# Kernel tuning notes

Measured on AMD Instinct MI355X. Metric: run time of the kernel, lower is better.

## Reference

```python
import jax, jax.numpy as jnp
import numpy as np

B = 500_000
N = 6          # n_neurons
STEPS = 10     # spiking update loop length
SUBSTEPS = 8   # TwoCompColumn substeps
NOISE_STD = 0.3
I_TONIC = -1.0
# Izhikevich 'RS' parameters
IZ_A, IZ_B, IZ_C, IZ_D = 0.02, 0.2, -65.0, 8.0
V_THRESH = 30.0
RATE_ALPHA = 0.1   # rate EMA
PC_TAU = 0.5       # compartment relaxation rate


def setup_inputs() -> dict:
    key = jax.random.key(0)
    k = jax.random.split(key, 8)
    heading = jax.random.normal(k[0], (B,), dtype=jnp.float32)
    speed = jax.random.uniform(k[1], (B,), dtype=jnp.float32)
    turn_rate = jax.random.normal(k[2], (B,), dtype=jnp.float32)
    predicted_turn = jax.random.normal(k[3], (B,), dtype=jnp.float32)
    predicted_speed = jax.random.uniform(k[4], (B,), dtype=jnp.float32)
    noise = jax.random.normal(k[5], (STEPS, B, N), dtype=jnp.float32)
    # Izhikevich resting state around v=-65, u=b*v, with small jitter
    v0 = -65.0 + 2.0 * jax.random.normal(k[6], (B, N), dtype=jnp.float32)
    u0 = IZ_B * v0
    rate0 = jnp.zeros((B, N), dtype=jnp.float32)
    return {
        "heading": heading, "speed": speed, "turn_rate": turn_rate,
        "predicted_turn": predicted_turn, "predicted_speed": predicted_speed,
        "noise": noise, "v0": v0, "u0": u0, "rate0": rate0,
    }


def reference(heading, speed, turn_rate, predicted_turn, predicted_speed,
              noise, v0, u0, rate0):
    # heading is carried for API fidelity; original forward never uses it.
    del heading
    tilt = jnp.minimum(1.0, jnp.abs(turn_rate) * speed * 0.5)          # [B]
    zero = jnp.float32(0.0)
    I = jnp.stack([
        jnp.maximum(zero, turn_rate) * 10.0,
        jnp.maximum(zero, -turn_rate) * 10.0,
        speed * 5.0,
        jnp.maximum(zero, -speed + 0.5) * 5.0,
        tilt * 8.0,
        tilt * 8.0,
    ], axis=-1)                                                        # [B, N]

    def izh_step(carry, nz):
        v, u, r = carry                                                # each [B, N]
        i_tot = I + nz * NOISE_STD + I_TONIC
        v = v + (0.04 * v * v + 5.0 * v + 140.0 - u + i_tot)
        u = u + IZ_A * (IZ_B * v - u)
        fired = v >= V_THRESH
        spk = fired.astype(v.dtype)
        v = jnp.where(fired, IZ_C, v)
        u = u + spk * IZ_D
        r = r * (1.0 - RATE_ALPHA) + spk * RATE_ALPHA
        return (v, u, r), None

    (_, _, rate), _ = jax.lax.scan(izh_step, (v0, u0, rate0), noise)
    rate_mean = jnp.mean(rate, axis=-1)                                # [B]

    # TwoCompColumn: basal tracks sensory, apical tracks prediction
    sensory = jnp.stack([turn_rate, speed], axis=-1)                   # [B, 2]
    prediction = jnp.stack([predicted_turn, predicted_speed], axis=-1) # [B, 2]

    def pc_step(carry, _):
        vb, va = carry
        vb = vb + PC_TAU * (sensory - vb)
        va = va + PC_TAU * (prediction - va)
        return (vb, va), None

    (vb, va), _ = jax.lax.scan(pc_step,
                               (jnp.zeros_like(sensory), jnp.zeros_like(prediction)),
                               None, length=SUBSTEPS)
    pe = vb - va                                                       # [B, 2]
    precision = 1.0 / (1.0 + pe * pe)                                  # [B, 2]
    free_energy = 0.5 * jnp.sum(precision * pe * pe, axis=-1)          # [B]
    pe_w = 0.7 * pe[..., 0] + 0.3 * pe[..., 1]                         # [B]
    prec_mean = jnp.mean(precision, axis=-1)                           # [B]
    postural = -prec_mean * pe_w * 0.3                                 # [B]

    # [B, 6]: (tilt, rate, postural_correction, prediction_error, precision, free_energy)
    return jnp.stack([tilt, rate_mean, postural, pe_w, prec_mean, free_energy], axis=-1)
```

## Files before the change

kernel.cpp:

```cpp
#include <hip/hip_runtime.h>

#define STEPS 10

__global__ __launch_bounds__(256) void spiking_vestibular_kernel(
    const float* __restrict__ speed,
    const float* __restrict__ turn_rate,
    const float* __restrict__ predicted_turn,
    const float* __restrict__ predicted_speed,
    const float* __restrict__ noise,
    const float* __restrict__ v0,
    const float* __restrict__ u0,
    const float* __restrict__ rate0,
    float* __restrict__ out,
    int B)
{
#pragma clang fp contract(off)
    int tid = blockIdx.x * blockDim.x + threadIdx.x;
    int b = tid >> 2;
    int g = tid & 3;
    if (b >= B) return;

    size_t base6 = (size_t)b * 6;
    int goff = (g == 3) ? 0 : (2 * g);

    float2 nz[STEPS];
#pragma unroll
    for (int t = 0; t < STEPS; ++t)
        nz[t] = *reinterpret_cast<const float2*>(noise + (size_t)t * (size_t)B * 6 + base6 + goff);

    float2 v2 = *reinterpret_cast<const float2*>(v0    + base6 + goff);
    float2 u2 = *reinterpret_cast<const float2*>(u0    + base6 + goff);
    float2 r2 = *reinterpret_cast<const float2*>(rate0 + base6 + goff);

    float tr = turn_rate[b];
    float sp = speed[b];
    float pt = predicted_turn[b];
    float ps = predicted_speed[b];

    float tilt = fminf(1.0f, (fabsf(tr) * sp) * 0.5f);

    float t8 = tilt * 8.0f;
    float Ia = (g == 0) ? fmaxf(0.0f, tr) * 10.0f
             : (g == 1) ? sp * 5.0f
             : t8;
    float Ib = (g == 0) ? fmaxf(0.0f, -tr) * 10.0f
             : (g == 1) ? fmaxf(0.0f, -sp + 0.5f) * 5.0f
             : t8;

    float va = v2.x, vb = v2.y;
    float ua = u2.x, ub = u2.y;
    float ra = r2.x, rb = r2.y;

#pragma unroll
    for (int t = 0; t < STEPS; ++t) {
        {
            float i_tot = Ia + nz[t].x * 0.3f + (-1.0f);
            float vv = va, un = ua;
            vv = vv + (((((0.04f * vv) * vv) + (5.0f * vv)) + 140.0f) - un + i_tot);
            un = un + 0.02f * ((0.2f * vv) - un);
            bool fired = (vv >= 30.0f);
            float spk = fired ? 1.0f : 0.0f;
            vv = fired ? -65.0f : vv;
            un = un + spk * 8.0f;
            ra = ra * 0.9f + spk * 0.1f;
            va = vv; ua = un;
        }
        {
            float i_tot = Ib + nz[t].y * 0.3f + (-1.0f);
            float vv = vb, un = ub;
            vv = vv + (((((0.04f * vv) * vv) + (5.0f * vv)) + 140.0f) - un + i_tot);
            un = un + 0.02f * ((0.2f * vv) - un);
            bool fired = (vv >= 30.0f);
            float spk = fired ? 1.0f : 0.0f;
            vv = fired ? -65.0f : vv;
            un = un + spk * 8.0f;
            rb = rb * 0.9f + spk * 0.1f;
            vb = vv; ub = un;
        }
    }

    float s  = ra + rb;
    float s1 = __shfl_down(s, 1, 4);
    float s2 = __shfl_down(s, 2, 4);
    float rate_mean = ((s + s1) + s2) / 6.0f;

    float cb0 = 0.0f, cb1 = 0.0f, ca0 = 0.0f, ca1 = 0.0f;
#pragma unroll
    for (int k = 0; k < 8; ++k) {
        cb0 = cb0 + 0.5f * (tr - cb0);
        cb1 = cb1 + 0.5f * (sp - cb1);
        ca0 = ca0 + 0.5f * (pt - ca0);
        ca1 = ca1 + 0.5f * (ps - ca1);
    }
    float pe0 = cb0 - ca0;
    float pe1 = cb1 - ca1;
    float prec0 = 1.0f / (1.0f + pe0 * pe0);
    float prec1 = 1.0f / (1.0f + pe1 * pe1);
    float fe = 0.5f * (((prec0 * pe0) * pe0) + ((prec1 * pe1) * pe1));
    float pe_w = 0.7f * pe0 + 0.3f * pe1;
    float prec_mean = (prec0 + prec1) / 2.0f;
    float postural = (-prec_mean) * pe_w * 0.3f;

    if (g < 3) {
        float2 o = (g == 0) ? make_float2(tilt, rate_mean)
                 : (g == 1) ? make_float2(postural, pe_w)
                 :            make_float2(prec_mean, fe);
        *reinterpret_cast<float2*>(out + base6 + 2 * g) = o;
    }
}

extern "C" void kernel_launch(void* const* d_in, const int* in_sizes, int n_in,
                              void* d_out, int out_size, void* d_ws, size_t ws_size,
                              hipStream_t stream) {
    const float* speed           = (const float*)d_in[1];
    const float* turn_rate       = (const float*)d_in[2];
    const float* predicted_turn  = (const float*)d_in[3];
    const float* predicted_speed = (const float*)d_in[4];
    const float* noise           = (const float*)d_in[5];
    const float* v0              = (const float*)d_in[6];
    const float* u0              = (const float*)d_in[7];
    const float* rate0           = (const float*)d_in[8];
    float* out                   = (float*)d_out;

    int B = in_sizes[1];
    long long total = (long long)B * 4;
    int block = 256;
    int grid = (int)((total + block - 1) / block);
    spiking_vestibular_kernel<<<grid, block, 0, stream>>>(
        speed, turn_rate, predicted_turn, predicted_speed,
        noise, v0, u0, rate0, out, B);
}
```

Measured before the change: 219.2 us.

## Stage noise and state slabs into LDS via direct global-to-LDS loads

```diff
diff --git a/kernel.cpp b/kernel.cpp
--- a/kernel.cpp
+++ b/kernel.cpp
@@ -1,6 +1,14 @@
 #include <hip/hip_runtime.h>
 
 #define STEPS 10
+#define EPB 64
+#define SLAB_FLOATS 384
+#define LDS_FLOATS 5120
+
+#define GLOAD_LDS16(gp, lp)                                            \
+    __builtin_amdgcn_global_load_lds(                                  \
+        (const __attribute__((address_space(1))) void*)(gp),           \
+        (__attribute__((address_space(3))) void*)(lp), 16, 0, 0)
 
 __global__ __launch_bounds__(256) void spiking_vestibular_kernel(
     const float* __restrict__ speed,
@@ -15,22 +23,51 @@
     int B)
 {
 #pragma clang fp contract(off)
-    int tid = blockIdx.x * blockDim.x + threadIdx.x;
-    int b = tid >> 2;
-    int g = tid & 3;
+    __shared__ float smem[LDS_FLOATS];
+
+    const int tid  = threadIdx.x;
+    const int wave = tid >> 6;
+    const int lane = tid & 63;
+    const long long b0 = (long long)blockIdx.x * EPB;
+
+    const long long nz_lim = (long long)STEPS * B * 6 - 4;
+    const long long st_lim = (long long)B * 6 - 4;
+
+#pragma unroll
+    for (int r = 0; r < 5; ++r) {
+        const int c = r * 4 + wave;
+        const int k = (c << 6) | lane;
+        int s = k / 96;
+        const int off16 = k - s * 96;
+        if (s > 12) s = 0;
+        const float* basep;
+        long long fidx, lim;
+        if (s < 10)       { basep = noise; fidx = ((long long)s * B + b0) * 6; lim = nz_lim; }
+        else if (s == 10) { basep = v0;    fidx = b0 * 6; lim = st_lim; }
+        else if (s == 11) { basep = u0;    fidx = b0 * 6; lim = st_lim; }
+        else              { basep = rate0; fidx = b0 * 6; lim = st_lim; }
+        fidx += (long long)off16 * 4;
+        if (fidx > lim) fidx = lim;
+        GLOAD_LDS16(basep + fidx, &smem[c * 256]);
+    }
+
+    __syncthreads();
+
+    const int e = tid >> 2;
+    const int g = tid & 3;
+    const long long b = b0 + e;
     if (b >= B) return;
 
-    size_t base6 = (size_t)b * 6;
-    int goff = (g == 3) ? 0 : (2 * g);
+    const int goff = (g == 3) ? 0 : (2 * g);
+    const int sb = e * 6 + goff;
 
-    float2 nz[STEPS];
+    float2 nzv[STEPS];
 #pragma unroll
     for (int t = 0; t < STEPS; ++t)
-        nz[t] = *reinterpret_cast<const float2*>(noise + (size_t)t * (size_t)B * 6 + base6 + goff);
-
-    float2 v2 = *reinterpret_cast<const float2*>(v0    + base6 + goff);
-    float2 u2 = *reinterpret_cast<const float2*>(u0    + base6 + goff);
-    float2 r2 = *reinterpret_cast<const float2*>(rate0 + base6 + goff);
+        nzv[t] = *reinterpret_cast<const float2*>(&smem[t * SLAB_FLOATS + sb]);
+    float2 v2 = *reinterpret_cast<const float2*>(&smem[10 * SLAB_FLOATS + sb]);
+    float2 u2 = *reinterpret_cast<const float2*>(&smem[11 * SLAB_FLOATS + sb]);
+    float2 r2 = *reinterpret_cast<const float2*>(&smem[12 * SLAB_FLOATS + sb]);
 
     float tr = turn_rate[b];
     float sp = speed[b];
@@ -54,7 +91,7 @@
 #pragma unroll
     for (int t = 0; t < STEPS; ++t) {
         {
-            float i_tot = Ia + nz[t].x * 0.3f + (-1.0f);
+            float i_tot = Ia + nzv[t].x * 0.3f + (-1.0f);
             float vv = va, un = ua;
             vv = vv + (((((0.04f * vv) * vv) + (5.0f * vv)) + 140.0f) - un + i_tot);
             un = un + 0.02f * ((0.2f * vv) - un);
@@ -66,7 +103,7 @@
             va = vv; ua = un;
         }
         {
-            float i_tot = Ib + nz[t].y * 0.3f + (-1.0f);
+            float i_tot = Ib + nzv[t].y * 0.3f + (-1.0f);
             float vv = vb, un = ub;
             vv = vv + (((((0.04f * vv) * vv) + (5.0f * vv)) + 140.0f) - un + i_tot);
             un = un + 0.02f * ((0.2f * vv) - un);
@@ -86,7 +123,7 @@
 
     float cb0 = 0.0f, cb1 = 0.0f, ca0 = 0.0f, ca1 = 0.0f;
 #pragma unroll
-    for (int k = 0; k < 8; ++k) {
+    for (int k2 = 0; k2 < 8; ++k2) {
         cb0 = cb0 + 0.5f * (tr - cb0);
         cb1 = cb1 + 0.5f * (sp - cb1);
         ca0 = ca0 + 0.5f * (pt - ca0);
@@ -105,7 +142,7 @@
         float2 o = (g == 0) ? make_float2(tilt, rate_mean)
                  : (g == 1) ? make_float2(postural, pe_w)
                  :            make_float2(prec_mean, fe);
-        *reinterpret_cast<float2*>(out + base6 + 2 * g) = o;
+        *reinterpret_cast<float2*>(out + (size_t)b * 6 + 2 * g) = o;
     }
 }
 
@@ -123,10 +160,8 @@
     float* out                   = (float*)d_out;
 
     int B = in_sizes[1];
-    long long total = (long long)B * 4;
-    int block = 256;
-    int grid = (int)((total + block - 1) / block);
-    spiking_vestibular_kernel<<<grid, block, 0, stream>>>(
+    int grid = (B + EPB - 1) / EPB;
+    spiking_vestibular_kernel<<<grid, 256, 0, stream>>>(
         speed, turn_rate, predicted_turn, predicted_speed,
         noise, v0, u0, rate0, out, B);
 }
```

Result: slower. 223.7 us (+2.1%).
